# Optimization experiments

Measured on AMD Instinct MI355X. Metric: run time of the kernel, lower is better.

The kernel has to match this reference:

```python
import jax, jax.numpy as jnp
import numpy as np

N = 50000      # nodes
E = 800000     # edges
F = 128        # num_features
DIM = 128      # dim
NF = 4         # n_factor
ND = DIM // NF # n_dim = 32
NL = 3         # n_layer
NC = 10        # n_class
G = 256        # num graphs in batch


def setup_inputs() -> dict:
    key = jax.random.key(0)
    ks = jax.random.split(key, 20)
    w = lambda k, shape, fan: (jax.random.normal(k, shape, jnp.float32) / np.sqrt(fan)).astype(jnp.float32)
    inp = {}
    inp["x"] = jax.random.normal(ks[0], (N, F), jnp.float32)
    inp["edge_index"] = jax.random.randint(ks[1], (2, E), 0, N)
    inp["batch"] = jnp.sort(jax.random.randint(ks[2], (N,), 0, G))
    # attention branch: lin0 (F->DIM) and att linear (2*DIM -> 1) per factor
    inp["lin0_W"] = w(ks[3], (NF, F, DIM), F)
    inp["lin0_b"] = jnp.zeros((NF, DIM), jnp.float32)
    inp["att_W"] = w(ks[4], (NF, 2 * DIM), 2 * DIM)
    inp["att_b"] = jnp.zeros((NF,), jnp.float32)
    # encoder per-factor input linear (F -> ND)
    inp["enc_W"] = w(ks[5], (NF, F, ND), F)
    inp["enc_b"] = jnp.zeros((NF, ND), jnp.float32)
    # GraphConv per factor/layer: lin_rel (with bias) + lin_root (no bias)
    inp["conv_Wrel"] = w(ks[6], (NF, NL, ND, ND), ND)
    inp["conv_brel"] = jnp.zeros((NF, NL, ND), jnp.float32)
    inp["conv_Wroot"] = w(ks[7], (NF, NL, ND, ND), ND)
    # GRU per factor (input ND, hidden ND), torch layout: [3*H, in]
    inp["gru_Wih"] = w(ks[8], (NF, 3 * ND, ND), ND)
    inp["gru_Whh"] = w(ks[9], (NF, 3 * ND, ND), ND)
    inp["gru_bih"] = jnp.zeros((NF, 3 * ND), jnp.float32)
    inp["gru_bhh"] = jnp.zeros((NF, 3 * ND), jnp.float32)
    # head
    inp["fc1_W"] = w(ks[10], (DIM, DIM), DIM)
    inp["fc1_b"] = jnp.zeros((DIM,), jnp.float32)
    inp["fc2_W"] = w(ks[11], (DIM, NC), DIM)
    inp["fc2_b"] = jnp.zeros((NC,), jnp.float32)
    return inp


def _gru_step(m, h, Wih, Whh, bih, bhh):
    # torch GRUCell math; gates order [r, z, n]
    gi = m @ Wih.T + bih   # [N, 3H]
    gh = h @ Whh.T + bhh
    ir, iz, inn = jnp.split(gi, 3, axis=-1)
    hr, hz, hn = jnp.split(gh, 3, axis=-1)
    r = jax.nn.sigmoid(ir + hr)
    z = jax.nn.sigmoid(iz + hz)
    n = jnp.tanh(inn + r * hn)
    return (1.0 - z) * n + z * h


def reference(x, edge_index, batch, lin0_W, lin0_b, att_W, att_b, enc_W, enc_b,
              conv_Wrel, conv_brel, conv_Wroot, gru_Wih, gru_Whh, gru_bih, gru_bhh,
              fc1_W, fc1_b, fc2_W, fc2_b):
    src, dst = edge_index[0], edge_index[1]
    counts = jnp.maximum(jax.ops.segment_sum(jnp.ones((N,), jnp.float32), batch, num_segments=G), 1.0)
    outs, atts = [], []
    for f in range(NF):
        # edge attention: sigmoid(6 * Linear([lin0(x[src]) || lin0(x[dst])]))
        a = x @ lin0_W[f] + lin0_b[f]                     # [N, DIM]
        Wl, Wr = att_W[f, :DIM], att_W[f, DIM:]
        e = a[src] @ Wl + a[dst] @ Wr + att_b[f]          # [E]
        att_i = jax.nn.sigmoid(6.0 * e)
        atts.append(att_i)
        # disentangled encoder for this factor
        out = x @ enc_W[f] + enc_b[f]                     # [N, ND]
        h = out
        for l in range(NL):
            # GraphConv: lin_rel(scatter_add(x[src]*w -> dst)) + lin_root(x)
            msg = out[src] * att_i[:, None]               # [E, ND]
            agg = jax.ops.segment_sum(msg, dst, num_segments=N)
            m = jax.nn.relu(agg @ conv_Wrel[f, l] + conv_brel[f, l] + out @ conv_Wroot[f, l])
            h = _gru_step(m, h, gru_Wih[f], gru_Whh[f], gru_bih[f], gru_bhh[f])
            out = h
        pooled = jax.ops.segment_sum(out, batch, num_segments=G) / counts[:, None]  # [G, ND]
        outs.append(pooled)
    out_cat = jnp.concatenate(outs, axis=-1)              # [G, DIM]
    pred = jax.nn.relu(out_cat @ fc1_W + fc1_b) @ fc2_W + fc2_b  # [G, NC]
    return pred, jnp.stack(atts, 0), jnp.stack(outs, 0)
```

## Files before the change

kernel.cpp:

```cpp
#include <hip/hip_runtime.h>
#include <hip/hip_fp16.h>
#include <math.h>

#define N   50000
#define E   800000
#define F   128
#define DIM 128
#define NF  4
#define ND  32
#define NL  3
#define NC  10
#define G   256
#define NB  196

typedef __attribute__((ext_vector_type(8))) short  s16x8;
typedef __attribute__((ext_vector_type(4))) float  f32x4;

__device__ __forceinline__ float sigm(float v) { return 1.0f / (1.0f + __expf(-v)); }

__device__ __forceinline__ unsigned int f2bf(float x) {
    unsigned int u = __float_as_uint(x);
    return (u + 0x7FFFu + ((u >> 16) & 1u)) >> 16;
}

__device__ __forceinline__ void split8(const float* v, s16x8& hi, s16x8& lo) {
    #pragma unroll
    for (int i = 0; i < 8; ++i) {
        float x = v[i];
        unsigned int h = f2bf(x);
        float hf = __uint_as_float(h << 16);
        hi[i] = (short)h;
        lo[i] = (short)f2bf(x - hf);
    }
}

#define MFMA(a, b, c) c = __builtin_amdgcn_mfma_f32_16x16x32_bf16(a, b, c, 0, 0, 0)
#define MF3(xh, xl, wh, wl, c) do { MFMA(xh, wh, c); MFMA(xh, wl, c); MFMA(xl, wh, c); } while (0)

__global__ void prep_kernel(const float* __restrict__ lin0_W, const float* __restrict__ lin0_b,
                            const float* __restrict__ att_W, const float* __restrict__ att_b,
                            float* __restrict__ vl, float* __restrict__ vr, float* __restrict__ cc) {
    int t = blockIdx.x * blockDim.x + threadIdx.x;
    if (t < NF * F) {
        int f = t >> 7, k = t & 127;
        const float* W  = lin0_W + (size_t)f * F * DIM + (size_t)k * DIM;
        const float* wl = att_W + f * 2 * DIM;
        const float* wr = wl + DIM;
        float sl = 0.f, sr = 0.f;
        for (int j = 0; j < DIM; ++j) { sl += W[j] * wl[j]; sr += W[j] * wr[j]; }
        vl[t] = sl; vr[t] = sr;
    }
    if (t < NF) {
        const float* b  = lin0_b + t * DIM;
        const float* wl = att_W + t * 2 * DIM;
        const float* wr = wl + DIM;
        float s = att_b[t];
        for (int j = 0; j < DIM; ++j) s += b[j] * (wl[j] + wr[j]);
        cc[t] = s;
    }
}

__global__ void wfrag_kernel(const float* __restrict__ Wrel, const float* __restrict__ Wroot,
                             const float* __restrict__ Wih, const float* __restrict__ Whh,
                             unsigned short* __restrict__ convfrag,
                             unsigned short* __restrict__ grufrag) {
    int b = blockIdx.x;
    int l = threadIdx.x;
    int lr = l & 15, lg = l >> 4;
    if (b < 12) {
        const float* wrelg  = Wrel  + (size_t)b * 1024;
        const float* wrootg = Wroot + (size_t)b * 1024;
        #pragma unroll
        for (int H = 0; H < 2; ++H) {
            #pragma unroll
            for (int i = 0; i < 8; ++i) {
                float x = wrelg[(lg * 8 + i) * 32 + H * 16 + lr];
                unsigned int h = f2bf(x);
                convfrag[(((size_t)b * 8 + 0 + H) * 64 + l) * 8 + i] = (unsigned short)h;
                convfrag[(((size_t)b * 8 + 2 + H) * 64 + l) * 8 + i] =
                    (unsigned short)f2bf(x - __uint_as_float(h << 16));
                x = wrootg[(lg * 8 + i) * 32 + H * 16 + lr];
                h = f2bf(x);
                convfrag[(((size_t)b * 8 + 4 + H) * 64 + l) * 8 + i] = (unsigned short)h;
                convfrag[(((size_t)b * 8 + 6 + H) * 64 + l) * 8 + i] =
                    (unsigned short)f2bf(x - __uint_as_float(h << 16));
            }
        }
    } else {
        int f = b - 12;
        const float* wihg = Wih + (size_t)f * 3072;
        const float* whhg = Whh + (size_t)f * 3072;
        #pragma unroll
        for (int m = 0; m < 6; ++m) {
            const float* base = (m < 3 ? wihg : whhg) + (size_t)((m % 3) * 32) * 32;
            #pragma unroll
            for (int H = 0; H < 2; ++H) {
                int col = H * 16 + lr;
                #pragma unroll
                for (int i = 0; i < 8; ++i) {
                    float x = base[(size_t)col * 32 + lg * 8 + i];
                    unsigned int h = f2bf(x);
                    grufrag[(((size_t)(f * 6 + m) * 4 + H) * 64 + l) * 8 + i] = (unsigned short)h;
                    grufrag[(((size_t)(f * 6 + m) * 4 + 2 + H) * 64 + l) * 8 + i] =
                        (unsigned short)f2bf(x - __uint_as_float(h << 16));
                }
            }
        }
    }
}

__global__ __launch_bounds__(256) void encode_kernel(
        const float* __restrict__ x, const float* __restrict__ enc_W,
        const float* __restrict__ enc_b,
        const float* __restrict__ vl, const float* __restrict__ vr,
        float* __restrict__ out, unsigned short* __restrict__ st16,
        float* __restrict__ alr) {
    int tid = threadIdx.x;
    int f = __builtin_amdgcn_readfirstlane(tid >> 6);
    int n = blockIdx.x * 64 + (tid & 63);
    int nc = n < N ? n : N - 1;
    const float* px  = x + (size_t)nc * F;
    const float* wf  = enc_W + (size_t)f * F * ND;
    const float* pvl = vl + f * F;
    const float* pvr = vr + f * F;
    const float* pb  = enc_b + f * ND;
    float acc[32];
    #pragma unroll
    for (int j = 0; j < 32; ++j) acc[j] = pb[j];
    float sl = 0.f, sr = 0.f;
    for (int k4 = 0; k4 < 32; ++k4) {
        float4 xv = *(const float4*)(px + k4 * 4);
        float xs[4] = {xv.x, xv.y, xv.z, xv.w};
        #pragma unroll
        for (int u = 0; u < 4; ++u) {
            int k = k4 * 4 + u;
            float xk = xs[u];
            const float* wrow = wf + k * 32;
            #pragma unroll
            for (int j = 0; j < 32; ++j) acc[j] = fmaf(xk, wrow[j], acc[j]);
            sl = fmaf(xk, pvl[k], sl);
            sr = fmaf(xk, pvr[k], sr);
        }
    }
    if (n < N) {
        float* po = out + (size_t)n * DIM + f * ND;
        #pragma unroll
        for (int q = 0; q < 8; ++q)
            *(float4*)(po + q * 4) = make_float4(acc[4*q], acc[4*q+1], acc[4*q+2], acc[4*q+3]);
        unsigned short* p16 = st16 + (size_t)n * DIM + f * ND;
        unsigned int pk[16];
        #pragma unroll
        for (int q = 0; q < 16; ++q)
            pk[q] = f2bf(acc[2*q]) | (f2bf(acc[2*q + 1]) << 16);
        uint4* o16 = (uint4*)p16;
        o16[0] = make_uint4(pk[0], pk[1], pk[2], pk[3]);
        o16[1] = make_uint4(pk[4], pk[5], pk[6], pk[7]);
        o16[2] = make_uint4(pk[8], pk[9], pk[10], pk[11]);
        o16[3] = make_uint4(pk[12], pk[13], pk[14], pk[15]);
        alr[(size_t)n * 8 + f]     = sl;
        alr[(size_t)n * 8 + 4 + f] = sr;
    }
}

__global__ void hist_kernel(const int* __restrict__ ei, int* __restrict__ deg) {
    int e = blockIdx.x * 256 + threadIdx.x;
    if (e < E) atomicAdd(&deg[ei[E + e]], 1);
}

__global__ void scan1_kernel(const int* __restrict__ deg, int* __restrict__ rowp,
                             int* __restrict__ bsum) {
    __shared__ int sh[256];
    int i = blockIdx.x * 256 + threadIdx.x;
    int v = (i < N) ? deg[i] : 0;
    sh[threadIdx.x] = v;
    __syncthreads();
    for (int off = 1; off < 256; off <<= 1) {
        int t = 0;
        if ((int)threadIdx.x >= off) t = sh[threadIdx.x - off];
        __syncthreads();
        sh[threadIdx.x] += t;
        __syncthreads();
    }
    if (i < N) rowp[i] = sh[threadIdx.x] - v;
    if (threadIdx.x == 255) bsum[blockIdx.x] = sh[255];
}

__global__ void scan2_kernel(int* __restrict__ bsum) {
    __shared__ int sh[256];
    int v = ((int)threadIdx.x < NB) ? bsum[threadIdx.x] : 0;
    sh[threadIdx.x] = v;
    __syncthreads();
    for (int off = 1; off < 256; off <<= 1) {
        int t = 0;
        if ((int)threadIdx.x >= off) t = sh[threadIdx.x - off];
        __syncthreads();
        sh[threadIdx.x] += t;
        __syncthreads();
    }
    if ((int)threadIdx.x < NB) bsum[threadIdx.x] = sh[threadIdx.x] - v;
}

__global__ void scan3_kernel(int* __restrict__ rowp, const int* __restrict__ bsum) {
    int i = blockIdx.x * 256 + threadIdx.x;
    if (i < N) rowp[i] += bsum[i >> 8];
}

__global__ void fill_kernel(const int* __restrict__ ei, const float* __restrict__ alr,
                            const float* __restrict__ cc,
                            const int* __restrict__ rowp, int* __restrict__ cnt,
                            uint4* __restrict__ erec, float* __restrict__ atts) {
    int e = blockIdx.x * 256 + threadIdx.x;
    if (e >= E) return;
    int s = ei[e];
    int d = ei[E + e];
    float4 al = *(const float4*)(alr + (size_t)s * 8);
    float4 ar = *(const float4*)(alr + (size_t)d * 8 + 4);
    float a0 = sigm(6.f * (al.x + ar.x + cc[0]));
    float a1 = sigm(6.f * (al.y + ar.y + cc[1]));
    float a2 = sigm(6.f * (al.z + ar.z + cc[2]));
    float a3 = sigm(6.f * (al.w + ar.w + cc[3]));
    atts[e]                 = a0;
    atts[(size_t)E + e]     = a1;
    atts[2 * (size_t)E + e] = a2;
    atts[3 * (size_t)E + e] = a3;
    unsigned int p01 = (unsigned int)__half_as_ushort(__float2half(a0))
                     | ((unsigned int)__half_as_ushort(__float2half(a1)) << 16);
    unsigned int p23 = (unsigned int)__half_as_ushort(__float2half(a2))
                     | ((unsigned int)__half_as_ushort(__float2half(a3)) << 16);
    int slot = rowp[d] + atomicAdd(&cnt[d], 1);
    erec[slot] = make_uint4((unsigned int)s, p01, p23, 0u);
}

__global__ __launch_bounds__(256) void gather_kernel(
        const uint4* __restrict__ erec,
        const int* __restrict__ rowp, const int* __restrict__ deg,
        const unsigned short* __restrict__ st16,
        unsigned int* __restrict__ agghi, unsigned int* __restrict__ agglo) {
    int gw = (blockIdx.x << 2) | ((int)threadIdx.x >> 6);
    int n = __builtin_amdgcn_readfirstlane(gw);
    int lane = threadIdx.x & 63;
    int f = lane >> 4;
    int beg = rowp[n];
    int cnt = deg[n];
    const unsigned char* rp = (const unsigned char*)(erec + beg);
    const int aoff = 4 + (f >> 1) * 4;
    const int ash  = (f & 1) * 16;
    const unsigned short* ob = st16 + lane * 2;
    float ax = 0.f, ay = 0.f;
    int i = 0;
    #define RECS(k)  (*(const int*)(rp + (size_t)(i + k) * 16))
    #define RECA(k)  __half2float(__ushort_as_half((unsigned short)( \
                        (*(const unsigned int*)(rp + (size_t)(i + k) * 16 + aoff)) >> ash)))
    for (; i + 8 <= cnt; i += 8) {
        int s0 = RECS(0), s1 = RECS(1), s2 = RECS(2), s3 = RECS(3);
        int s4 = RECS(4), s5 = RECS(5), s6 = RECS(6), s7 = RECS(7);
        float a0 = RECA(0), a1 = RECA(1), a2 = RECA(2), a3 = RECA(3);
        float a4 = RECA(4), a5 = RECA(5), a6 = RECA(6), a7 = RECA(7);
        unsigned int u0 = *(const unsigned int*)(ob + (size_t)s0 * DIM);
        unsigned int u1 = *(const unsigned int*)(ob + (size_t)s1 * DIM);
        unsigned int u2 = *(const unsigned int*)(ob + (size_t)s2 * DIM);
        unsigned int u3 = *(const unsigned int*)(ob + (size_t)s3 * DIM);
        unsigned int u4 = *(const unsigned int*)(ob + (size_t)s4 * DIM);
        unsigned int u5 = *(const unsigned int*)(ob + (size_t)s5 * DIM);
        unsigned int u6 = *(const unsigned int*)(ob + (size_t)s6 * DIM);
        unsigned int u7 = *(const unsigned int*)(ob + (size_t)s7 * DIM);
        ax += a0 * __uint_as_float(u0 << 16) + a1 * __uint_as_float(u1 << 16)
            + a2 * __uint_as_float(u2 << 16) + a3 * __uint_as_float(u3 << 16)
            + a4 * __uint_as_float(u4 << 16) + a5 * __uint_as_float(u5 << 16)
            + a6 * __uint_as_float(u6 << 16) + a7 * __uint_as_float(u7 << 16);
        ay += a0 * __uint_as_float(u0 & 0xFFFF0000u) + a1 * __uint_as_float(u1 & 0xFFFF0000u)
            + a2 * __uint_as_float(u2 & 0xFFFF0000u) + a3 * __uint_as_float(u3 & 0xFFFF0000u)
            + a4 * __uint_as_float(u4 & 0xFFFF0000u) + a5 * __uint_as_float(u5 & 0xFFFF0000u)
            + a6 * __uint_as_float(u6 & 0xFFFF0000u) + a7 * __uint_as_float(u7 & 0xFFFF0000u);
    }
    for (; i + 4 <= cnt; i += 4) {
        int s0 = RECS(0), s1 = RECS(1), s2 = RECS(2), s3 = RECS(3);
        float a0 = RECA(0), a1 = RECA(1), a2 = RECA(2), a3 = RECA(3);
        unsigned int u0 = *(const unsigned int*)(ob + (size_t)s0 * DIM);
        unsigned int u1 = *(const unsigned int*)(ob + (size_t)s1 * DIM);
        unsigned int u2 = *(const unsigned int*)(ob + (size_t)s2 * DIM);
        unsigned int u3 = *(const unsigned int*)(ob + (size_t)s3 * DIM);
        ax += a0 * __uint_as_float(u0 << 16) + a1 * __uint_as_float(u1 << 16)
            + a2 * __uint_as_float(u2 << 16) + a3 * __uint_as_float(u3 << 16);
        ay += a0 * __uint_as_float(u0 & 0xFFFF0000u) + a1 * __uint_as_float(u1 & 0xFFFF0000u)
            + a2 * __uint_as_float(u2 & 0xFFFF0000u) + a3 * __uint_as_float(u3 & 0xFFFF0000u);
    }
    for (; i < cnt; ++i) {
        int s = RECS(0);
        float a = RECA(0);
        unsigned int u = *(const unsigned int*)(ob + (size_t)s * DIM);
        ax += a * __uint_as_float(u << 16);
        ay += a * __uint_as_float(u & 0xFFFF0000u);
    }
    #undef RECS
    #undef RECA
    unsigned int hx = f2bf(ax), hy = f2bf(ay);
    float fx = __uint_as_float(hx << 16), fy = __uint_as_float(hy << 16);
    agghi[(size_t)n * 64 + lane] = hx | (hy << 16);
    agglo[(size_t)n * 64 + lane] = f2bf(ax - fx) | (f2bf(ay - fy) << 16);
}

__global__ __launch_bounds__(256) void update_kernel(
        const unsigned int* __restrict__ agghi, const unsigned int* __restrict__ agglo,
        float* __restrict__ out, unsigned short* __restrict__ st16,
        const unsigned short* __restrict__ convfrag, const unsigned short* __restrict__ grufrag,
        const float* __restrict__ brel,
        const float* __restrict__ bih, const float* __restrict__ bhh, int lay) {
    __shared__ __align__(16) unsigned short mls[NF][2][2][16 * 40];
    int tid = threadIdx.x;
    int f   = __builtin_amdgcn_readfirstlane(tid >> 6);
    int l   = tid & 63;
    int lr  = l & 15;
    int lg  = l >> 4;
    int node0 = blockIdx.x * 32;

    const unsigned short* cf = convfrag + (size_t)(f * NL + lay) * 8 * 64 * 8;
    s16x8 wrelh[2], wrell[2], wrooth[2], wrootl[2];
    #pragma unroll
    for (int H = 0; H < 2; ++H) {
        wrelh[H]  = *(const s16x8*)&cf[((0 + H) * 64 + l) * 8];
        wrell[H]  = *(const s16x8*)&cf[((2 + H) * 64 + l) * 8];
        wrooth[H] = *(const s16x8*)&cf[((4 + H) * 64 + l) * 8];
        wrootl[H] = *(const s16x8*)&cf[((6 + H) * 64 + l) * 8];
    }
    const unsigned short* gf = grufrag + (size_t)f * 6 * 4 * 64 * 8;
    s16x8 wirh[2], wirl[2], wizh[2], wizl[2], winh[2], winl[2];
    s16x8 whrh[2], whrl[2], whzh[2], whzl[2], whnh[2], whnl[2];
    #pragma unroll
    for (int H = 0; H < 2; ++H) {
        wirh[H] = *(const s16x8*)&gf[((0 * 4 + H) * 64 + l) * 8];
        wirl[H] = *(const s16x8*)&gf[((0 * 4 + 2 + H) * 64 + l) * 8];
        wizh[H] = *(const s16x8*)&gf[((1 * 4 + H) * 64 + l) * 8];
        wizl[H] = *(const s16x8*)&gf[((1 * 4 + 2 + H) * 64 + l) * 8];
        winh[H] = *(const s16x8*)&gf[((2 * 4 + H) * 64 + l) * 8];
        winl[H] = *(const s16x8*)&gf[((2 * 4 + 2 + H) * 64 + l) * 8];
        whrh[H] = *(const s16x8*)&gf[((3 * 4 + H) * 64 + l) * 8];
        whrl[H] = *(const s16x8*)&gf[((3 * 4 + 2 + H) * 64 + l) * 8];
        whzh[H] = *(const s16x8*)&gf[((4 * 4 + H) * 64 + l) * 8];
        whzl[H] = *(const s16x8*)&gf[((4 * 4 + 2 + H) * 64 + l) * 8];
        whnh[H] = *(const s16x8*)&gf[((5 * 4 + H) * 64 + l) * 8];
        whnl[H] = *(const s16x8*)&gf[((5 * 4 + 2 + H) * 64 + l) * 8];
    }

    float br_[2], bir_[2], biz_[2], bin_[2], bhn_[2];
    #pragma unroll
    for (int H = 0; H < 2; ++H) {
        int c = H * 16 + lr;
        br_[H]  = brel[(f * NL + lay) * 32 + c];
        bir_[H] = bih[f * 96 + c]      + bhh[f * 96 + c];
        biz_[H] = bih[f * 96 + 32 + c] + bhh[f * 96 + 32 + c];
        bin_[H] = bih[f * 96 + 64 + c];
        bhn_[H] = bhh[f * 96 + 64 + c];
    }

    const unsigned short* ahp = (const unsigned short*)agghi;
    const unsigned short* alp = (const unsigned short*)agglo;

    #pragma unroll
    for (int s = 0; s < 2; ++s) {
        int n0 = node0 + s * 16;
        unsigned short* mHi = &mls[f][s][0][0];
        unsigned short* mLo = &mls[f][s][1][0];
        int na  = n0 + lr;
        int nac = na < N ? na : N - 1;
        s16x8 aggH = *(const s16x8*)&ahp[(size_t)nac * DIM + f * ND + lg * 8];
        s16x8 aggL = *(const s16x8*)&alp[(size_t)nac * DIM + f * ND + lg * 8];
        const float* ph = out + (size_t)nac * DIM + f * ND + lg * 8;
        float vh[8];
        { float4 q0 = *(const float4*)ph, q1 = *(const float4*)(ph + 4);
          vh[0]=q0.x; vh[1]=q0.y; vh[2]=q0.z; vh[3]=q0.w; vh[4]=q1.x; vh[5]=q1.y; vh[6]=q1.z; vh[7]=q1.w; }
        s16x8 hH, hL;
        split8(vh, hH, hL);
        float hj0[4], hj1[4];
        #pragma unroll
        for (int j = 0; j < 4; ++j) {
            int nn_ = n0 + lg * 4 + j;
            int nnc = nn_ < N ? nn_ : N - 1;
            hj0[j] = out[(size_t)nnc * DIM + f * ND + lr];
            hj1[j] = out[(size_t)nnc * DIM + f * ND + 16 + lr];
        }

        f32x4 c0 = {br_[0], br_[0], br_[0], br_[0]};
        f32x4 c1 = {br_[1], br_[1], br_[1], br_[1]};
        MF3(aggH, aggL, wrelh[0],  wrell[0],  c0);
        MF3(hH,   hL,   wrooth[0], wrootl[0], c0);
        MF3(aggH, aggL, wrelh[1],  wrell[1],  c1);
        MF3(hH,   hL,   wrooth[1], wrootl[1], c1);

        #pragma unroll
        for (int j = 0; j < 4; ++j) {
            int row = lg * 4 + j;
            float v0 = fmaxf(c0[j], 0.f);
            float v1 = fmaxf(c1[j], 0.f);
            unsigned int h0 = f2bf(v0);
            unsigned int h1 = f2bf(v1);
            mHi[row * 40 + lr]      = (unsigned short)h0;
            mHi[row * 40 + 16 + lr] = (unsigned short)h1;
            mLo[row * 40 + lr]      = (unsigned short)f2bf(v0 - __uint_as_float(h0 << 16));
            mLo[row * 40 + 16 + lr] = (unsigned short)f2bf(v1 - __uint_as_float(h1 << 16));
        }
        __asm__ volatile("s_waitcnt lgkmcnt(0)" ::: "memory");
        __builtin_amdgcn_sched_barrier(0x37);
        s16x8 mH = *(const s16x8*)&mHi[lr * 40 + lg * 8];
        s16x8 mL = *(const s16x8*)&mLo[lr * 40 + lg * 8];

        f32x4 gr0 = {bir_[0], bir_[0], bir_[0], bir_[0]};
        f32x4 gr1 = {bir_[1], bir_[1], bir_[1], bir_[1]};
        f32x4 gz0 = {biz_[0], biz_[0], biz_[0], biz_[0]};
        f32x4 gz1 = {biz_[1], biz_[1], biz_[1], biz_[1]};
        f32x4 gn0 = {bin_[0], bin_[0], bin_[0], bin_[0]};
        f32x4 gn1 = {bin_[1], bin_[1], bin_[1], bin_[1]};
        f32x4 gh0 = {bhn_[0], bhn_[0], bhn_[0], bhn_[0]};
        f32x4 gh1 = {bhn_[1], bhn_[1], bhn_[1], bhn_[1]};
        MF3(mH, mL, wirh[0], wirl[0], gr0);  MF3(hH, hL, whrh[0], whrl[0], gr0);
        MF3(mH, mL, wirh[1], wirl[1], gr1);  MF3(hH, hL, whrh[1], whrl[1], gr1);
        MF3(mH, mL, wizh[0], wizl[0], gz0);  MF3(hH, hL, whzh[0], whzl[0], gz0);
        MF3(mH, mL, wizh[1], wizl[1], gz1);  MF3(hH, hL, whzh[1], whzl[1], gz1);
        MF3(mH, mL, winh[0], winl[0], gn0);
        MF3(mH, mL, winh[1], winl[1], gn1);
        MF3(hH, hL, whnh[0], whnl[0], gh0);
        MF3(hH, hL, whnh[1], whnl[1], gh1);

        #pragma unroll
        for (int j = 0; j < 4; ++j) {
            int n = n0 + lg * 4 + j;
            float r0 = sigm(gr0[j]);
            float z0 = sigm(gz0[j]);
            float t0 = 2.f * sigm(2.f * (gn0[j] + r0 * gh0[j])) - 1.f;
            float res0 = (1.f - z0) * t0 + z0 * hj0[j];
            float r1 = sigm(gr1[j]);
            float z1 = sigm(gz1[j]);
            float t1 = 2.f * sigm(2.f * (gn1[j] + r1 * gh1[j])) - 1.f;
            float res1 = (1.f - z1) * t1 + z1 * hj1[j];
            if (n < N) {
                out[(size_t)n * DIM + f * ND + lr]       = res0;
                out[(size_t)n * DIM + f * ND + 16 + lr]  = res1;
                st16[(size_t)n * DIM + f * ND + lr]      = (unsigned short)f2bf(res0);
                st16[(size_t)n * DIM + f * ND + 16 + lr] = (unsigned short)f2bf(res1);
            }
        }
    }
}

__global__ void goff_kernel(const int* __restrict__ batch, int* __restrict__ goff) {
    int g = threadIdx.x;
    int lo = 0, hi = N;
    while (lo < hi) {
        int mid = (lo + hi) >> 1;
        if (batch[mid] < g) lo = mid + 1; else hi = mid;
    }
    goff[g] = lo;
    if (g == 0) goff[G] = N;
}

__global__ void pool_kernel(const float* __restrict__ st, const int* __restrict__ goff,
                            float* __restrict__ pooled, float* __restrict__ outsout) {
    __shared__ float acc2[128];
    int g = blockIdx.x;
    int c = threadIdx.x & 127;
    int half = threadIdx.x >> 7;
    int beg = goff[g], cnt = goff[g + 1] - beg;
    float acc = 0.f;
    for (int i = half; i < cnt; i += 2) acc += st[(size_t)(beg + i) * DIM + c];
    if (half == 1) acc2[c] = acc;
    __syncthreads();
    if (half == 0) {
        float tot = acc + acc2[c];
        float val = tot / fmaxf((float)cnt, 1.0f);
        pooled[g * DIM + c] = val;
        int f = c >> 5, d = c & 31;
        outsout[((size_t)f * G + g) * ND + d] = val;
    }
}

__global__ void mlp_kernel(const float* __restrict__ pooled,
                           const float* __restrict__ fc1_W, const float* __restrict__ fc1_b,
                           const float* __restrict__ fc2_W, const float* __restrict__ fc2_b,
                           float* __restrict__ pred) {
    __shared__ float row[DIM], hid[DIM];
    int g = blockIdx.x, c = threadIdx.x;
    row[c] = pooled[(size_t)g * DIM + c];
    __syncthreads();
    float acc = fc1_b[c];
    #pragma unroll 8
    for (int k = 0; k < DIM; ++k) acc += row[k] * fc1_W[k * DIM + c];
    hid[c] = fmaxf(acc, 0.f);
    __syncthreads();
    if (c < NC) {
        float p = fc2_b[c];
        for (int k = 0; k < DIM; ++k) p += hid[k] * fc2_W[k * NC + c];
        pred[(size_t)g * NC + c] = p;
    }
}

extern "C" void kernel_launch(void* const* d_in, const int* in_sizes, int n_in,
                              void* d_out, int out_size, void* d_ws, size_t ws_size,
                              hipStream_t stream) {
    const float* x         = (const float*)d_in[0];
    const int*   ei        = (const int*)  d_in[1];
    const int*   batch     = (const int*)  d_in[2];
    const float* lin0_W    = (const float*)d_in[3];
    const float* lin0_b    = (const float*)d_in[4];
    const float* att_W     = (const float*)d_in[5];
    const float* att_b     = (const float*)d_in[6];
    const float* enc_W     = (const float*)d_in[7];
    const float* enc_b     = (const float*)d_in[8];
    const float* conv_Wrel = (const float*)d_in[9];
    const float* conv_brel = (const float*)d_in[10];
    const float* conv_Wroot= (const float*)d_in[11];
    const float* gru_Wih   = (const float*)d_in[12];
    const float* gru_Whh   = (const float*)d_in[13];
    const float* gru_bih   = (const float*)d_in[14];
    const float* gru_bhh   = (const float*)d_in[15];
    const float* fc1_W     = (const float*)d_in[16];
    const float* fc1_b     = (const float*)d_in[17];
    const float* fc2_W     = (const float*)d_in[18];
    const float* fc2_b     = (const float*)d_in[19];

    float* outp    = (float*)d_out;
    float* pred    = outp;
    float* atts    = outp + G * NC;
    float* outsout = atts + (size_t)NF * E;

    float* fp     = (float*)d_ws;
    float* st     = fp;                   fp += (size_t)N * DIM;
    unsigned int* agghi = (unsigned int*)fp;     fp += (size_t)N * 64;
    unsigned int* agglo = (unsigned int*)fp;     fp += (size_t)N * 64;
    unsigned short* st16 = (unsigned short*)fp;  fp += (size_t)N * DIM / 2;
    float* alr    = fp;                   fp += (size_t)N * 8;
    float* vl     = fp;                   fp += NF * F;
    float* vr     = fp;                   fp += NF * F;
    float* cc     = fp;                   fp += 4;
    float* pooled = fp;                   fp += G * DIM;
    unsigned short* convfrag = (unsigned short*)fp;  fp += 12 * 8 * 64 * 8 / 2;
    unsigned short* grufrag  = (unsigned short*)fp;  fp += 4 * 24 * 64 * 8 / 2;
    uint4* erec  = (uint4*)fp;            fp += (size_t)NF * E;
    int* ip    = (int*)fp;
    int* deg   = ip;                      ip += N;
    int* cnt   = ip;                      ip += N;
    int* rowp  = ip;                      ip += N;
    int* bsum  = ip;                      ip += 256;
    int* goff  = ip;                      ip += G + 1;

    hipMemsetAsync(deg, 0, (size_t)(2 * N) * sizeof(int), stream);

    prep_kernel<<<2, 256, 0, stream>>>(lin0_W, lin0_b, att_W, att_b, vl, vr, cc);
    wfrag_kernel<<<16, 64, 0, stream>>>(conv_Wrel, conv_Wroot, gru_Wih, gru_Whh,
                                        convfrag, grufrag);
    goff_kernel<<<1, 256, 0, stream>>>(batch, goff);
    encode_kernel<<<(N + 63) / 64, 256, 0, stream>>>(x, enc_W, enc_b, vl, vr, st, st16, alr);

    hist_kernel<<<(E + 255) / 256, 256, 0, stream>>>(ei, deg);
    scan1_kernel<<<NB, 256, 0, stream>>>(deg, rowp, bsum);
    scan2_kernel<<<1, 256, 0, stream>>>(bsum);
    scan3_kernel<<<NB, 256, 0, stream>>>(rowp, bsum);
    fill_kernel<<<(E + 255) / 256, 256, 0, stream>>>(ei, alr, cc, rowp, cnt, erec, atts);

    for (int l = 0; l < NL; ++l) {
        gather_kernel<<<N / 4, 256, 0, stream>>>(erec, rowp, deg, st16, agghi, agglo);
        update_kernel<<<(N + 31) / 32, 256, 0, stream>>>(agghi, agglo, st, st16,
                                                         convfrag, grufrag, conv_brel,
                                                         gru_bih, gru_bhh, l);
    }

    pool_kernel<<<G, 256, 0, stream>>>(st, goff, pooled, outsout);
    mlp_kernel<<<G, DIM, 0, stream>>>(pooled, fc1_W, fc1_b, fc2_W, fc2_b, pred);
}
```

Baseline: 480.7 us.

## Move encoder projection onto split-bf16 MFMA with prepacked weight fragments

Replaces the scalar FMA encode kernel (one thread per node per factor, 32 accumulators) with a matrix-core version that splits x and the encoder/attention weights into bf16 hi/lo pairs and uses three-term MFMA products to keep near-fp32 accuracy. The encoder and attention projection vectors are packed into fragment layout inside the existing weight-fragment kernel, which gains four blocks. Each encode block now processes 32 nodes per factor, and outputs are written as scattered scalar stores instead of vector stores. The three-pass bf16 split adds rounding error and some conversion work on x in exchange for offloading the FLOPs to MFMA.

```diff
diff --git a/kernel.cpp b/kernel.cpp
--- a/kernel.cpp
+++ b/kernel.cpp
@@ -62,8 +62,12 @@
 
 __global__ void wfrag_kernel(const float* __restrict__ Wrel, const float* __restrict__ Wroot,
                              const float* __restrict__ Wih, const float* __restrict__ Whh,
+                             const float* __restrict__ enc_W,
+                             const float* __restrict__ vl, const float* __restrict__ vr,
                              unsigned short* __restrict__ convfrag,
-                             unsigned short* __restrict__ grufrag) {
+                             unsigned short* __restrict__ grufrag,
+                             unsigned short* __restrict__ encfrag,
+                             unsigned short* __restrict__ attfrag) {
     int b = blockIdx.x;
     int l = threadIdx.x;
     int lr = l & 15, lg = l >> 4;
@@ -86,7 +90,7 @@
                     (unsigned short)f2bf(x - __uint_as_float(h << 16));
             }
         }
-    } else {
+    } else if (b < 16) {
         int f = b - 12;
         const float* wihg = Wih + (size_t)f * 3072;
         const float* whhg = Whh + (size_t)f * 3072;
@@ -106,59 +110,94 @@
                 }
             }
         }
+    } else {
+        int f = b - 16;
+        const float* we = enc_W + (size_t)f * F * ND;
+        #pragma unroll
+        for (int c = 0; c < 4; ++c) {
+            #pragma unroll
+            for (int i = 0; i < 8; ++i) {
+                int k = c * 32 + lg * 8 + i;
+                #pragma unroll
+                for (int H = 0; H < 2; ++H) {
+                    float x = we[(size_t)k * 32 + H * 16 + lr];
+                    unsigned int h = f2bf(x);
+                    encfrag[((((size_t)(f * 4 + c) * 2 + H) * 2 + 0) * 64 + l) * 8 + i] =
+                        (unsigned short)h;
+                    encfrag[((((size_t)(f * 4 + c) * 2 + H) * 2 + 1) * 64 + l) * 8 + i] =
+                        (unsigned short)f2bf(x - __uint_as_float(h << 16));
+                }
+                float av = (lr == 0) ? vl[f * F + k] : (lr == 1) ? vr[f * F + k] : 0.f;
+                unsigned int ha = f2bf(av);
+                attfrag[(((size_t)(f * 4 + c) * 2 + 0) * 64 + l) * 8 + i] = (unsigned short)ha;
+                attfrag[(((size_t)(f * 4 + c) * 2 + 1) * 64 + l) * 8 + i] =
+                    (unsigned short)f2bf(av - __uint_as_float(ha << 16));
+            }
+        }
     }
 }
 
 __global__ __launch_bounds__(256) void encode_kernel(
-        const float* __restrict__ x, const float* __restrict__ enc_W,
+        const float* __restrict__ x,
+        const unsigned short* __restrict__ encfrag,
+        const unsigned short* __restrict__ attfrag,
         const float* __restrict__ enc_b,
-        const float* __restrict__ vl, const float* __restrict__ vr,
         float* __restrict__ out, unsigned short* __restrict__ st16,
         float* __restrict__ alr) {
     int tid = threadIdx.x;
-    int f = __builtin_amdgcn_readfirstlane(tid >> 6);
-    int n = blockIdx.x * 64 + (tid & 63);
-    int nc = n < N ? n : N - 1;
-    const float* px  = x + (size_t)nc * F;
-    const float* wf  = enc_W + (size_t)f * F * ND;
-    const float* pvl = vl + f * F;
-    const float* pvr = vr + f * F;
-    const float* pb  = enc_b + f * ND;
-    float acc[32];
+    int f  = __builtin_amdgcn_readfirstlane(tid >> 6);
+    int l  = tid & 63;
+    int lr = l & 15, lg = l >> 4;
+    int node0 = blockIdx.x * 32;
+
+    s16x8 beh[4][2], bel[4][2], bah[4], bal[4];
     #pragma unroll
-    for (int j = 0; j < 32; ++j) acc[j] = pb[j];
-    float sl = 0.f, sr = 0.f;
-    for (int k4 = 0; k4 < 32; ++k4) {
-        float4 xv = *(const float4*)(px + k4 * 4);
-        float xs[4] = {xv.x, xv.y, xv.z, xv.w};
-        #pragma unroll
-        for (int u = 0; u < 4; ++u) {
-            int k = k4 * 4 + u;
-            float xk = xs[u];
-            const float* wrow = wf + k * 32;
-            #pragma unroll
-            for (int j = 0; j < 32; ++j) acc[j] = fmaf(xk, wrow[j], acc[j]);
-            sl = fmaf(xk, pvl[k], sl);
-            sr = fmaf(xk, pvr[k], sr);
-        }
-    }
-    if (n < N) {
-        float* po = out + (size_t)n * DIM + f * ND;
-        #pragma unroll
-        for (int q = 0; q < 8; ++q)
-            *(float4*)(po + q * 4) = make_float4(acc[4*q], acc[4*q+1], acc[4*q+2], acc[4*q+3]);
-        unsigned short* p16 = st16 + (size_t)n * DIM + f * ND;
-        unsigned int pk[16];
-        #pragma unroll
-        for (int q = 0; q < 16; ++q)
-            pk[q] = f2bf(acc[2*q]) | (f2bf(acc[2*q + 1]) << 16);
-        uint4* o16 = (uint4*)p16;
-        o16[0] = make_uint4(pk[0], pk[1], pk[2], pk[3]);
-        o16[1] = make_uint4(pk[4], pk[5], pk[6], pk[7]);
-        o16[2] = make_uint4(pk[8], pk[9], pk[10], pk[11]);
-        o16[3] = make_uint4(pk[12], pk[13], pk[14], pk[15]);
-        alr[(size_t)n * 8 + f]     = sl;
-        alr[(size_t)n * 8 + 4 + f] = sr;
+    for (int c = 0; c < 4; ++c) {
+        #pragma unroll
+        for (int H = 0; H < 2; ++H) {
+            beh[c][H] = *(const s16x8*)&encfrag[((((size_t)(f*4 + c)*2 + H)*2 + 0)*64 + l)*8];
+            bel[c][H] = *(const s16x8*)&encfrag[((((size_t)(f*4 + c)*2 + H)*2 + 1)*64 + l)*8];
+        }
+        bah[c] = *(const s16x8*)&attfrag[(((size_t)(f*4 + c)*2 + 0)*64 + l)*8];
+        bal[c] = *(const s16x8*)&attfrag[(((size_t)(f*4 + c)*2 + 1)*64 + l)*8];
+    }
+    float be0 = enc_b[f*32 + lr], be1 = enc_b[f*32 + 16 + lr];
+
+    #pragma unroll
+    for (int s = 0; s < 2; ++s) {
+        int n0 = node0 + s * 16;
+        int na = n0 + lr; int nac = na < N ? na : N - 1;
+        const float* px = x + (size_t)nac * F + lg * 8;
+        s16x8 xh[4], xl[4];
+        #pragma unroll
+        for (int c = 0; c < 4; ++c) {
+            float v[8];
+            float4 q0 = *(const float4*)(px + c * 32);
+            float4 q1 = *(const float4*)(px + c * 32 + 4);
+            v[0]=q0.x; v[1]=q0.y; v[2]=q0.z; v[3]=q0.w; v[4]=q1.x; v[5]=q1.y; v[6]=q1.z; v[7]=q1.w;
+            split8(v, xh[c], xl[c]);
+        }
+        f32x4 o0 = {be0, be0, be0, be0};
+        f32x4 o1 = {be1, be1, be1, be1};
+        f32x4 ca = {0.f, 0.f, 0.f, 0.f};
+        #pragma unroll
+        for (int c = 0; c < 4; ++c) {
+            MF3(xh[c], xl[c], beh[c][0], bel[c][0], o0);
+            MF3(xh[c], xl[c], beh[c][1], bel[c][1], o1);
+            MF3(xh[c], xl[c], bah[c],    bal[c],    ca);
+        }
+        #pragma unroll
+        for (int j = 0; j < 4; ++j) {
+            int n = n0 + lg * 4 + j;
+            if (n < N) {
+                out[(size_t)n * DIM + f * ND + lr]       = o0[j];
+                out[(size_t)n * DIM + f * ND + 16 + lr]  = o1[j];
+                st16[(size_t)n * DIM + f * ND + lr]      = (unsigned short)f2bf(o0[j]);
+                st16[(size_t)n * DIM + f * ND + 16 + lr] = (unsigned short)f2bf(o1[j]);
+                if (lr == 0)      alr[(size_t)n * 8 + f]     = ca[j];
+                else if (lr == 1) alr[(size_t)n * 8 + 4 + f] = ca[j];
+            }
+        }
     }
 }
 
@@ -534,6 +573,8 @@
     float* pooled = fp;                   fp += G * DIM;
     unsigned short* convfrag = (unsigned short*)fp;  fp += 12 * 8 * 64 * 8 / 2;
     unsigned short* grufrag  = (unsigned short*)fp;  fp += 4 * 24 * 64 * 8 / 2;
+    unsigned short* encfrag  = (unsigned short*)fp;  fp += 4 * 16 * 64 * 8 / 2;
+    unsigned short* attfrag  = (unsigned short*)fp;  fp += 4 * 8 * 64 * 8 / 2;
     uint4* erec  = (uint4*)fp;            fp += (size_t)NF * E;
     int* ip    = (int*)fp;
     int* deg   = ip;                      ip += N;
@@ -545,10 +586,12 @@
     hipMemsetAsync(deg, 0, (size_t)(2 * N) * sizeof(int), stream);
 
     prep_kernel<<<2, 256, 0, stream>>>(lin0_W, lin0_b, att_W, att_b, vl, vr, cc);
-    wfrag_kernel<<<16, 64, 0, stream>>>(conv_Wrel, conv_Wroot, gru_Wih, gru_Whh,
-                                        convfrag, grufrag);
+    wfrag_kernel<<<20, 64, 0, stream>>>(conv_Wrel, conv_Wroot, gru_Wih, gru_Whh,
+                                        enc_W, vl, vr,
+                                        convfrag, grufrag, encfrag, attfrag);
     goff_kernel<<<1, 256, 0, stream>>>(batch, goff);
-    encode_kernel<<<(N + 63) / 64, 256, 0, stream>>>(x, enc_W, enc_b, vl, vr, st, st16, alr);
+    encode_kernel<<<(N + 31) / 32, 256, 0, stream>>>(x, encfrag, attfrag, enc_b,
+                                                     st, st16, alr);
 
     hist_kernel<<<(E + 255) / 256, 256, 0, stream>>>(ei, deg);
     scan1_kernel<<<NB, 256, 0, stream>>>(deg, rowp, bsum);
```

After: 475.2 us. Within noise of the previous version (-1.2%).
